# Kernel tuning notes

Measured on AMD Instinct MI355X. Metric: run time of the kernel, lower is better.

## Reference

```python
import jax, jax.numpy as jnp
import numpy as np

B, T, D = 4, 256, 1024
H, G = 512, 8
P, N, L = 384, 384, 16


def setup_inputs() -> dict:
    key = jax.random.key(0)
    ks = jax.random.split(key, 16)
    feats = jax.random.normal(ks[0], (B, T, D), jnp.float32)
    vid_idx = jnp.arange(P, dtype=jnp.int32) // (P // B)          # sorted, 96 proposals per video
    starts = jax.random.randint(ks[1], (P,), 0, T - L)
    gather_idx = jax.random.permutation(ks[2], P).astype(jnp.int32)
    block_id = jnp.repeat(jnp.arange(N // 32, dtype=jnp.int32), 32)  # 12 event sequences of 32
    s = jax.random.uniform(ks[3], (N,), minval=0.0, maxval=80.0)
    e = s + jax.random.uniform(ks[4], (N,), minval=1.0, maxval=20.0)
    timestamps = jnp.stack([s, e], axis=1)
    durations = jnp.full((N,), 120.0, jnp.float32)

    def lin(k, fi, fo):
        return jax.random.normal(k, (fi, fo), jnp.float32) / np.sqrt(fi).astype(np.float32)

    return dict(
        feats=feats, vid_idx=vid_idx, starts=starts, clip_len=L,
        gather_idx=gather_idx, block_id=block_id, timestamps=timestamps, durations=durations,
        W_pre=lin(ks[5], D, H), b_pre=jnp.zeros((H,), jnp.float32),
        W_q=lin(ks[6], H, H), b_q=jnp.zeros((H,), jnp.float32),
        W_k=lin(ks[7], H, H), b_k=jnp.zeros((H,), jnp.float32),
        W_v=lin(ks[8], H, H), b_v=jnp.zeros((H,), jnp.float32),
        W_p1=lin(ks[9], H, H), b_p1=jnp.zeros((H,), jnp.float32),
        W_p2=lin(ks[10], H, G), b_p2=jnp.zeros((G,), jnp.float32),
    )


def reference(feats, vid_idx, starts, clip_len, gather_idx, block_id, timestamps, durations,
              W_pre, b_pre, W_q, b_q, W_k, b_k, W_v, b_v, W_p1, b_p1, W_p2, b_p2):
    dt = feats.dtype
    # --- get_clip_level_feats: fixed clip_len spans -> vectorized gather ---
    t_idx = starts[:, None] + jnp.arange(clip_len)                # (P, L)
    clip_feats = feats[vid_idx[:, None], t_idx]                   # (P, L, D)
    clip_mask = jnp.ones((P, clip_len), dt)
    event_feats = clip_feats.sum(1) / (clip_mask.sum(1, keepdims=True) + 1e-5)
    # pre_map (dropout = identity in eval)
    ef = jax.nn.relu(event_feats @ W_pre + b_pre)                 # (P, H)
    # expand proposals into event rows; block-diagonal sequence mask
    X = ef[gather_idx]                                            # (N, H)
    mask = (block_id[:, None] == block_id[None, :]).astype(dt)[None]  # (1, N, N)
    # grouped scaled-dot attention
    Hg = H // G
    q = (X @ W_q + b_q).reshape(N, G, Hg).transpose(1, 0, 2)      # (G, N, Hg)
    k = (X @ W_k + b_k).reshape(N, G, Hg).transpose(1, 0, 2)
    v = (X @ W_v + b_v).reshape(N, G, Hg).transpose(1, 0, 2)
    cos_sim = jnp.einsum('gnd,gmd->gnm', q, k) / np.float32(np.sqrt(Hg))
    # --- positional relation branch ---
    st, en = timestamps[:, 0:1], timestamps[:, 1:2]               # (N, 1)
    center = 0.5 * (st + en)
    length = jnp.maximum(en - st, 0.1)
    delta_center = (center - center.T) / length                  # (N, N)
    delta_length = jnp.log(length.T / length)
    pos_mat = jnp.stack([delta_center, delta_length], axis=2)    # (N, N, 2)
    feat_range = jnp.arange(H // 4, dtype=dt)
    dim_mat = jnp.float32(10000.0) ** (4.0 / H * feat_range)      # (H/4,)
    div = (100.0 * pos_mat)[..., None] / dim_mat                  # (N, N, 2, H/4)
    pe = jnp.concatenate([jnp.sin(div), jnp.cos(div)], axis=-1).reshape(N, N, H)
    pos_sim = jnp.tanh(pe @ W_p1 + b_p1) @ W_p2 + b_p2            # (N, N, G)
    sim = cos_sim + pos_sim.transpose(2, 0, 1)                    # (G, N, N)
    sim = jax.nn.softmax(sim, axis=2)
    sim = sim * mask / (1e-5 + jnp.sum(sim * mask, axis=2, keepdims=True))
    ctx = jnp.einsum('gnm,gmd->gnd', sim, v).transpose(1, 0, 2).reshape(N, H)
    ctx = jnp.concatenate([jax.nn.relu(ctx), X], axis=1)          # (N, 2H)
    # 100-dim temporal occupancy indicator
    s_idx = jnp.minimum((timestamps[:, 0] / durations * 99).astype(jnp.int32), 99)
    e_idx = jnp.minimum((timestamps[:, 1] / durations * 99).astype(jnp.int32), 99)
    ar = jnp.arange(100)
    pos_ind = ((ar >= s_idx[:, None]) & (ar <= e_idx[:, None])).astype(dt)
    event_ctx = jnp.concatenate([ctx, pos_ind], axis=1)           # (N, 2H+100)
    return (event_ctx, clip_feats, clip_mask)
```

## Files before the change

### kernel.cpp

```cpp
#include <hip/hip_runtime.h>
#include <hip/hip_bf16.h>

#define NN 384
#define NP 147456

using short8 = __attribute__((ext_vector_type(8))) short;
using f32x4  = __attribute__((ext_vector_type(4))) float;

#define DEV static __device__ __forceinline__

DEV unsigned short f2b(float f){
  unsigned int u = __float_as_uint(f);
  u += 0x7FFFu + ((u >> 16) & 1u);
  return (unsigned short)(u >> 16);
}
DEV unsigned int pk2(float lo, float hi){
  __hip_bfloat162 h = __float22bfloat162_rn(make_float2(lo, hi));
  union { __hip_bfloat162 b; unsigned int u; } c; c.b = h; return c.u;
}
DEV float exp_e(float x){ return __builtin_amdgcn_exp2f(x * 1.4426950408889634f); }
DEV float tanh_f(float x){
  float e = exp_e(2.0f * x);
  return 1.0f - 2.0f * __builtin_amdgcn_rcpf(e + 1.0f);
}

typedef const void __attribute__((address_space(1)))* gas_ptr;
typedef void       __attribute__((address_space(3)))* las_ptr;
DEV void gload16(const void* g, void* l){
  __builtin_amdgcn_global_load_lds((gas_ptr)g, (las_ptr)l, 16, 0, 0);
}

DEV int frag_off(int r, int lane){
  return r * 64 + ((((lane >> 4) ^ ((r >> 1) & 3)) & 3) << 4);
}

__global__ __launch_bounds__(256) void setup_kernel(
    const float* __restrict__ feats, const int* __restrict__ vid_idx,
    const int* __restrict__ starts, float* __restrict__ outClip,
    float* __restrict__ outMask, unsigned short* __restrict__ evb,
    const float* __restrict__ Wpre, const float* __restrict__ Wq,
    const float* __restrict__ Wk,   const float* __restrict__ Wv,
    const float* __restrict__ W1,   const float* __restrict__ W2,
    const float* __restrict__ bq,   const float* __restrict__ bk,
    const float* __restrict__ bv,
    unsigned short* __restrict__ WTpre, unsigned short* __restrict__ WTqkv,
    unsigned short* __restrict__ W1F,   unsigned short* __restrict__ W2F,
    float* __restrict__ bqkv)
{
  __shared__ float tile[64][65];
  int bid = blockIdx.x, tid = threadIdx.x;
  if(bid < 384){
    int p = bid;
    int vid = vid_idx[p], st = starts[p];
    const float4* base = (const float4*)feats + ((long)vid * 256 + st) * 256;
    float4* oc = (float4*)outClip + (long)p * 16 * 256;
    float4 acc = make_float4(0.f, 0.f, 0.f, 0.f);
#pragma unroll
    for(int l = 0; l < 16; ++l){
      float4 v = base[l * 256 + tid];
      oc[l * 256 + tid] = v;
      acc.x += v.x; acc.y += v.y; acc.z += v.z; acc.w += v.w;
    }
    float den = 16.0f + 1e-5f;
    unsigned short* d = evb + (long)p * 1024 + tid * 4;
    d[0] = f2b(acc.x / den); d[1] = f2b(acc.y / den);
    d[2] = f2b(acc.z / den); d[3] = f2b(acc.w / den);
    if(tid < 16) outMask[p * 16 + tid] = 1.0f;
    return;
  }
  int id = bid - 384;
  if(id == 384){
    for(int i = tid; i < 8192; i += 256){
      int kk = i >> 9, l = (i >> 3) & 63, e = i & 7;
      int k = kk * 32 + ((l >> 4) << 3) + e, g = l & 15;
      W2F[i] = (g < 8) ? f2b(W2[k * 8 + g]) : (unsigned short)0;
    }
    for(int i = tid; i < 512; i += 256){
      bqkv[i] = bq[i]; bqkv[512 + i] = bk[i]; bqkv[1024 + i] = bv[i];
    }
    return;
  }
  if(id >= 320){
    int base = (id - 320) * 4096;
#pragma unroll
    for(int j = 0; j < 16; ++j){
      int i = base + j * 256 + tid;
      int e = i & 7, l = (i >> 3) & 63, cbkk = i >> 9;
      int cb = cbkk & 31, kk = cbkk >> 5;
      int k = kk * 32 + ((l >> 4) << 3) + e;
      int col = cb * 16 + (l & 15);
      W1F[i] = f2b(W1[(long)k * 512 + col]);
    }
    return;
  }
  const float* src; unsigned short* dst; int K, C, k0, c0;
  if(id < 128){ src = Wpre; dst = WTpre; K = 1024; C = 512;
                k0 = (id >> 3) * 64; c0 = (id & 7) * 64; }
  else { int l = id - 128; int which = l >> 6; int r = l & 63;
         src = which == 0 ? Wq : (which == 1 ? Wk : Wv);
         dst = WTqkv + which * 512 * 512; K = 512; C = 512;
         k0 = (r >> 3) * 64; c0 = (r & 7) * 64; }
#pragma unroll
  for(int i = 0; i < 16; ++i){
    int idx = tid + i * 256, r = idx >> 6, c = idx & 63;
    tile[r][c] = src[(long)(k0 + r) * C + c0 + c];
  }
  __syncthreads();
#pragma unroll
  for(int i = 0; i < 16; ++i){
    int idx = tid + i * 256, r = idx >> 6, c = idx & 63;
    dst[(long)(c0 + r) * K + k0 + c] = f2b(tile[c][r]);
  }
}

template<int NI>
__global__ __launch_bounds__(256, 1) void gemmN(
    const unsigned short* __restrict__ A, const int* __restrict__ gidx,
    const unsigned short* __restrict__ BT, const float* __restrict__ bias,
    float* __restrict__ Cf, unsigned short* __restrict__ Cb,
    float* __restrict__ kT, int K, int ldc, int relu)
{
  __shared__ unsigned short sA[4][64 * 32];
  __shared__ unsigned short sB[4][64 * NI * 32];
  const int tid = threadIdx.x, lane = tid & 63, w = tid >> 6;
  const int r0 = blockIdx.x * 64, c0 = blockIdx.y * (64 * NI);
  const int nk = K >> 5;

  int rA = w * 16 + (lane >> 2);
  int gsltA = (lane & 3) ^ ((rA >> 1) & 3);
  int arow = gidx ? gidx[r0 + rA] : (r0 + rA);
  const unsigned short* srcA = A + (long)arow * K + gsltA * 8;

  const unsigned short* srcB[NI];
#pragma unroll
  for(int i = 0; i < NI; ++i){
    int rB = (w * NI + i) * 16 + (lane >> 2);
    srcB[i] = BT + (long)(c0 + rB) * K + (((lane & 3) ^ ((rB >> 1) & 3)) * 8);
  }

  auto STAGE = [&](int kk){
    int buf = kk & 3, ko = kk * 32;
#pragma unroll
    for(int i = 0; i < NI; ++i)
      gload16(srcB[i] + ko, (char*)sB[buf] + (w * NI + i) * 1024);
    gload16(srcA + ko, (char*)sA[buf] + w * 1024);
  };

  f32x4 acc[4][NI];
#pragma unroll
  for(int i = 0; i < 4; ++i)
#pragma unroll
    for(int j = 0; j < NI; ++j) acc[i][j] = (f32x4){0.f, 0.f, 0.f, 0.f};

  STAGE(0); STAGE(1); STAGE(2);

  for(int kk = 0; kk < nk; ++kk){
    int cur = kk & 3;
    if constexpr(NI == 1){
      if(kk < nk - 2)       asm volatile("s_waitcnt vmcnt(4)" ::: "memory");
      else if(kk == nk - 2) asm volatile("s_waitcnt vmcnt(2)" ::: "memory");
      else                  asm volatile("s_waitcnt vmcnt(0)" ::: "memory");
    } else {
      if(kk < nk - 2)       asm volatile("s_waitcnt vmcnt(6)" ::: "memory");
      else if(kk == nk - 2) asm volatile("s_waitcnt vmcnt(3)" ::: "memory");
      else                  asm volatile("s_waitcnt vmcnt(0)" ::: "memory");
    }
    __builtin_amdgcn_s_barrier();

    short8 af[4], bfv[NI];
#pragma unroll
    for(int mi = 0; mi < 4; ++mi)
      af[mi] = *(const short8*)((const char*)sA[cur] + frag_off(mi * 16 + (lane & 15), lane));
#pragma unroll
    for(int ni = 0; ni < NI; ++ni)
      bfv[ni] = *(const short8*)((const char*)sB[cur] + frag_off(w * 16 * NI + ni * 16 + (lane & 15), lane));

    if(kk + 3 < nk) STAGE(kk + 3);

#pragma unroll
    for(int mi = 0; mi < 4; ++mi)
#pragma unroll
      for(int ni = 0; ni < NI; ++ni)
        acc[mi][ni] = __builtin_amdgcn_mfma_f32_16x16x32_bf16(af[mi], bfv[ni], acc[mi][ni], 0, 0, 0);
  }

#pragma unroll
  for(int ni = 0; ni < NI; ++ni){
    int c = c0 + w * 16 * NI + ni * 16 + (lane & 15);
    float bv = bias ? bias[c] : 0.f;
#pragma unroll
    for(int mi = 0; mi < 4; ++mi){
      int rbase = r0 + mi * 16 + ((lane >> 4) << 2);
      float4 kv4;
#pragma unroll
      for(int r = 0; r < 4; ++r){
        float v = acc[mi][ni][r] + bv;
        if(relu) v = fmaxf(v, 0.f);
        Cf[(long)(rbase + r) * ldc + c] = v;
        if(Cb) Cb[(long)(rbase + r) * ldc + c] = f2b(v);
        ((float*)&kv4)[r] = v;
      }
      if(kT && c >= 512 && c < 1024)
        *(float4*)(kT + (long)(c - 512) * 384 + rbase) = kv4;
    }
  }
}

__global__ __launch_bounds__(512, 1) void pos_sim_kernel(
    const unsigned short* __restrict__ W1F, const float* __restrict__ b1,
    const unsigned short* __restrict__ W2F, const float* __restrict__ b2,
    const float* __restrict__ ts, float* __restrict__ simc)
{
  __shared__ unsigned short peA[16][2048];
  const int tid = threadIdx.x, lane = tid & 63, w = tid >> 6;
  const int jt = tid & 7, prow = tid >> 3;
  const int swzp = (prow >> 1) & 3;

  float wj[16];
#pragma unroll
  for(int u = 0; u < 16; ++u)
    wj[u] = __builtin_amdgcn_exp2f(-0.10381025296523f * (float)(jt * 16 + u));
  float b1v[4];
#pragma unroll
  for(int ni = 0; ni < 4; ++ni) b1v[ni] = b1[w * 64 + ni * 16 + (lane & 15)];
  const float b2v = b2[lane & 7];
  const float inv2pi = 0.15915494309189535f;

  const int p0 = blockIdx.x * 64;

  {
    int q = p0 + prow;
    int n = q >> 5;
    int m = ((n >> 5) << 5) + (q & 31);
    float sn = ts[2*n], en = ts[2*n+1], sm = ts[2*m], em = ts[2*m+1];
    float cn = 0.5f*(sn+en), cm = 0.5f*(sm+em);
    float ln = fmaxf(en-sn, 0.1f), lm = fmaxf(em-sm, 0.1f);
    float a = 100.0f * (cn - cm) / ln;
    float b = 100.0f * 0.69314718055994531f * __builtin_amdgcn_logf(lm / ln);
#pragma unroll
    for(int half = 0; half < 2; ++half){
      unsigned int pa[4], pb[4], pc[4], pd[4];
#pragma unroll
      for(int up = 0; up < 4; ++up){
        int u0 = half * 8 + up * 2;
        float ra0 = __builtin_amdgcn_fractf(a * wj[u0]     * inv2pi);
        float ra1 = __builtin_amdgcn_fractf(a * wj[u0 + 1] * inv2pi);
        float rb0 = __builtin_amdgcn_fractf(b * wj[u0]     * inv2pi);
        float rb1 = __builtin_amdgcn_fractf(b * wj[u0 + 1] * inv2pi);
        pa[up] = pk2(__builtin_amdgcn_sinf(ra0), __builtin_amdgcn_sinf(ra1));
        pb[up] = pk2(__builtin_amdgcn_cosf(ra0), __builtin_amdgcn_cosf(ra1));
        pc[up] = pk2(__builtin_amdgcn_sinf(rb0), __builtin_amdgcn_sinf(rb1));
        pd[up] = pk2(__builtin_amdgcn_cosf(rb0), __builtin_amdgcn_cosf(rb1));
      }
      int s0 = (((jt & 1) * 2 + half) ^ swzp);
      char* base = (char*)&peA[0][0] + prow * 64 + (s0 << 4);
      int ch = jt >> 1;
      *(uint4*)(base + (ch     ) * 4096) = make_uint4(pa[0], pa[1], pa[2], pa[3]);
      *(uint4*)(base + (ch +  4) * 4096) = make_uint4(pb[0], pb[1], pb[2], pb[3]);
      *(uint4*)(base + (ch +  8) * 4096) = make_uint4(pc[0], pc[1], pc[2], pc[3]);
      *(uint4*)(base + (ch + 12) * 4096) = make_uint4(pd[0], pd[1], pd[2], pd[3]);
    }
  }
  asm volatile("s_waitcnt lgkmcnt(0)" ::: "memory");
  __builtin_amdgcn_s_barrier();

  f32x4 acc[4][4];
#pragma unroll
  for(int i = 0; i < 4; ++i)
#pragma unroll
    for(int j = 0; j < 4; ++j) acc[i][j] = (f32x4){0.f, 0.f, 0.f, 0.f};

  for(int kk = 0; kk < 16; ++kk){
    short8 af[4], bfv[4];
#pragma unroll
    for(int ni = 0; ni < 4; ++ni)
      bfv[ni] = *(const short8*)(W1F + (((kk * 32 + (w * 4 + ni)) * 64 + lane) << 3));
#pragma unroll
    for(int mi = 0; mi < 4; ++mi)
      af[mi] = *(const short8*)((const char*)&peA[kk][0] + frag_off(mi * 16 + (lane & 15), lane));
    __builtin_amdgcn_s_setprio(1);
#pragma unroll
    for(int mi = 0; mi < 4; ++mi)
#pragma unroll
      for(int ni = 0; ni < 4; ++ni)
        acc[mi][ni] = __builtin_amdgcn_mfma_f32_16x16x32_bf16(af[mi], bfv[ni], acc[mi][ni], 0, 0, 0);
    __builtin_amdgcn_s_setprio(0);
  }
  asm volatile("s_waitcnt lgkmcnt(0)" ::: "memory");
  __builtin_amdgcn_s_barrier();

#pragma unroll
  for(int ni = 0; ni < 4; ++ni){
    int h = w * 64 + ni * 16 + (lane & 15);
    int ch = h >> 5;
    int kb = (h & 31) * 2;
#pragma unroll
    for(int mi = 0; mi < 4; ++mi){
#pragma unroll
      for(int r = 0; r < 4; ++r){
        int row = mi * 16 + ((lane >> 4) << 2) + r;
        float tv = tanh_f(acc[mi][ni][r] + b1v[ni]);
        *(unsigned short*)((char*)&peA[ch][0] + row * 64 + (kb ^ (((row >> 1) & 3) << 4))) = f2b(tv);
      }
    }
  }
  asm volatile("s_waitcnt lgkmcnt(0)" ::: "memory");
  __builtin_amdgcn_s_barrier();

  if(w < 4){
    f32x4 acc2 = (f32x4){0.f, 0.f, 0.f, 0.f};
    for(int kk = 0; kk < 16; ++kk){
      short8 af2  = *(const short8*)((const char*)&peA[kk][0] + frag_off(w * 16 + (lane & 15), lane));
      short8 w2fk = *(const short8*)(W2F + ((kk * 64 + lane) << 3));
      acc2 = __builtin_amdgcn_mfma_f32_16x16x32_bf16(af2, w2fk, acc2, 0, 0, 0);
    }
    if((lane & 15) < 8){
      int g = lane & 15;
      int rbase = w * 16 + ((lane >> 4) << 2);
#pragma unroll
      for(int r = 0; r < 4; ++r)
        simc[(long)g * 12288 + p0 + rbase + r] = acc2[r] + b2v;
    }
  }
}

__global__ __launch_bounds__(512) void attn_tail_kernel(
    const float* __restrict__ simc, const float* __restrict__ qkv,
    const float* __restrict__ kT,
    const float* __restrict__ ef, const int* __restrict__ gidx,
    const float* __restrict__ ts, const float* __restrict__ dur,
    float* __restrict__ out)
{
  int n = blockIdx.x, tid = threadIdx.x, g = tid >> 6, lane = tid & 63;
  __shared__ float qs[8][64];
  __shared__ float w32s[8][32];
  qs[g][lane] = qkv[(long)n * 1536 + g * 64 + lane];
  __syncthreads();

  const float* srow = simc + (long)g * 12288 + (long)n * 32;
  int m0 = (n >> 5) << 5;

  float sv[6], e[6], mx = -1e30f;
#pragma unroll
  for(int i = 0; i < 6; ++i){
    int m = lane + i * 64;
    const float* kc = kT + (long)g * 24576 + m;
    float s = 0.f;
#pragma unroll 8
    for(int d = 0; d < 64; ++d)
      s = fmaf(qs[g][d], kc[(long)d * 384], s);
    float sc = (m >= m0 && m < m0 + 32) ? srow[m - m0] : 0.0f;
    sv[i] = s * 0.125f + sc;
    mx = fmaxf(mx, sv[i]);
  }
#pragma unroll
  for(int o = 32; o > 0; o >>= 1) mx = fmaxf(mx, __shfl_xor(mx, o));
  float Z = 0.f;
#pragma unroll
  for(int i = 0; i < 6; ++i){ e[i] = exp_e(sv[i] - mx); Z += e[i]; }
#pragma unroll
  for(int o = 32; o > 0; o >>= 1) Z += __shfl_xor(Z, o);
  float ms = 0.f;
#pragma unroll
  for(int i = 0; i < 6; ++i){ int m = lane + i * 64; if(m >= m0 && m < m0 + 32) ms += e[i]; }
#pragma unroll
  for(int o = 32; o > 0; o >>= 1) ms += __shfl_xor(ms, o);
  float inv = 1.0f / (1e-5f * Z + ms);
#pragma unroll
  for(int i = 0; i < 6; ++i){ int m = lane + i * 64; if(m >= m0 && m < m0 + 32) w32s[g][m - m0] = e[i] * inv; }
  __syncthreads();
  float a = 0.f;
#pragma unroll 8
  for(int j = 0; j < 32; ++j)
    a = fmaf(w32s[g][j], qkv[(long)(m0 + j) * 1536 + 1024 + g * 64 + lane], a);
  out[(long)n * 1124 + g * 64 + lane] = fmaxf(a, 0.f);

  int pidx = gidx[n];
  out[(long)n * 1124 + 512 + tid] = ef[(long)pidx * 512 + tid];
  if(tid < 100){
    float d = dur[n];
    int si = (int)(ts[2 * n]     / d * 99.0f); si = min(si, 99);
    int ei = (int)(ts[2 * n + 1] / d * 99.0f); ei = min(ei, 99);
    out[(long)n * 1124 + 1024 + tid] = (tid >= si && tid <= ei) ? 1.0f : 0.0f;
  }
}

extern "C" void kernel_launch(void* const* d_in, const int* in_sizes, int n_in,
                              void* d_out, int out_size, void* d_ws, size_t ws_size,
                              hipStream_t stream)
{
  const float* feats   = (const float*)d_in[0];
  const int*   vid_idx = (const int*)d_in[1];
  const int*   starts  = (const int*)d_in[2];
  const int*   gidx    = (const int*)d_in[4];
  const float* ts      = (const float*)d_in[6];
  const float* dur     = (const float*)d_in[7];
  const float* W_pre   = (const float*)d_in[8];
  const float* b_pre   = (const float*)d_in[9];
  const float* W_q     = (const float*)d_in[10];
  const float* b_q     = (const float*)d_in[11];
  const float* W_k     = (const float*)d_in[12];
  const float* b_k     = (const float*)d_in[13];
  const float* W_v     = (const float*)d_in[14];
  const float* b_v     = (const float*)d_in[15];
  const float* W_p1    = (const float*)d_in[16];
  const float* b_p1    = (const float*)d_in[17];
  const float* W_p2    = (const float*)d_in[18];
  const float* b_p2    = (const float*)d_in[19];

  float* out     = (float*)d_out;
  float* outClip = out + 431616;
  float* outMask = out + 6723072;

  char* ws = (char*)d_ws;
  size_t off = 0;
  auto alloc = [&](size_t bytes){ void* p = ws + off; off = (off + bytes + 255) & ~(size_t)255; return p; };
  unsigned short* evb   = (unsigned short*)alloc(384 * 1024 * 2);
  unsigned short* WTpre = (unsigned short*)alloc(512 * 1024 * 2);
  unsigned short* WTqkv = (unsigned short*)alloc((size_t)1536 * 512 * 2);
  unsigned short* W1F   = (unsigned short*)alloc(262144 * 2);
  unsigned short* W2F   = (unsigned short*)alloc(8192 * 2);
  float*  bqkv = (float*)alloc(1536 * 4);
  float*  ef   = (float*)alloc(384 * 512 * 4);
  unsigned short* efb = (unsigned short*)alloc(384 * 512 * 2);
  float*  qkv  = (float*)alloc((size_t)384 * 1536 * 4);
  float*  kT   = (float*)alloc((size_t)512 * 384 * 4);
  float*  simc = (float*)alloc((size_t)8 * 12288 * 4);

  setup_kernel<<<dim3(769), dim3(256), 0, stream>>>(
      feats, vid_idx, starts, outClip, outMask, evb,
      W_pre, W_q, W_k, W_v, W_p1, W_p2, b_q, b_k, b_v,
      WTpre, WTqkv, W1F, W2F, bqkv);
  gemmN<1><<<dim3(6, 8), dim3(256), 0, stream>>>(evb, (const int*)nullptr, WTpre, b_pre, ef, efb, (float*)nullptr, 1024, 512, 1);
  gemmN<1><<<dim3(6, 24), dim3(256), 0, stream>>>(efb, gidx, WTqkv, bqkv, qkv, (unsigned short*)nullptr, kT, 512, 1536, 0);
  pos_sim_kernel<<<dim3(192), dim3(512), 0, stream>>>(W1F, b_p1, W2F, b_p2, ts, simc);
  attn_tail_kernel<<<dim3(384), dim3(512), 0, stream>>>(simc, qkv, kT, ef, gidx, ts, dur, out);
}
```

Measured before the change: 79.58 us.

## Fuse positional-similarity MLP into attention tail kernel per query row

Merges pos_sim_kernel into attn_tail_kernel. Each of the 384 blocks now computes the sin/cos positional encodings and the two-layer tanh MLP for its own 32 block-local pairs in shared memory, then uses the scores straight from LDS. This removes one kernel launch and the global simc round trip. The cost is that each block now does 32-row MFMA tiles instead of 64-row ones, with half the waves idle in the second GEMM, and it keeps launch_bounds(512,1), which may limit occupancy of the attention part.

```diff
diff --git a/kernel.cpp b/kernel.cpp
--- a/kernel.cpp
+++ b/kernel.cpp
@@ -2,7 +2,6 @@
 #include <hip/hip_bf16.h>
 
 #define NN 384
-#define NP 147456
 
 using short8 = __attribute__((ext_vector_type(8))) short;
 using f32x4  = __attribute__((ext_vector_type(4))) float;
@@ -206,81 +205,84 @@
   }
 }
 
-__global__ __launch_bounds__(512, 1) void pos_sim_kernel(
+__global__ __launch_bounds__(512, 1) void attn_tail_kernel(
     const unsigned short* __restrict__ W1F, const float* __restrict__ b1,
     const unsigned short* __restrict__ W2F, const float* __restrict__ b2,
-    const float* __restrict__ ts, float* __restrict__ simc)
+    const float* __restrict__ qkv,  const float* __restrict__ kT,
+    const float* __restrict__ ef,   const int* __restrict__ gidx,
+    const float* __restrict__ ts,   const float* __restrict__ dur,
+    float* __restrict__ out)
 {
-  __shared__ unsigned short peA[16][2048];
-  const int tid = threadIdx.x, lane = tid & 63, w = tid >> 6;
-  const int jt = tid & 7, prow = tid >> 3;
-  const int swzp = (prow >> 1) & 3;
-
-  float wj[16];
-#pragma unroll
-  for(int u = 0; u < 16; ++u)
-    wj[u] = __builtin_amdgcn_exp2f(-0.10381025296523f * (float)(jt * 16 + u));
+  __shared__ char  peB[32768];
+  __shared__ float qs[8][64];
+  __shared__ float w32s[8][32];
+  __shared__ float scoreS[32][8];
+
+  const int n = blockIdx.x, tid = threadIdx.x;
+  const int g = tid >> 6, lane = tid & 63, w = tid >> 6, l15 = lane & 15;
+  const int m0 = (n >> 5) << 5;
+  const float kexp = -0.10381025296523f;
+  const float inv2pi = 0.15915494309189535f;
+
+  auto peAt = [&](int ch) -> char* { return peB + ch * 2048; };
+
+  qs[g][lane] = qkv[(long)n * 1536 + g * 64 + lane];
+
   float b1v[4];
 #pragma unroll
-  for(int ni = 0; ni < 4; ++ni) b1v[ni] = b1[w * 64 + ni * 16 + (lane & 15)];
-  const float b2v = b2[lane & 7];
-  const float inv2pi = 0.15915494309189535f;
-
-  const int p0 = blockIdx.x * 64;
+  for(int ni = 0; ni < 4; ++ni) b1v[ni] = b1[w * 64 + ni * 16 + l15];
 
   {
-    int q = p0 + prow;
-    int n = q >> 5;
-    int m = ((n >> 5) << 5) + (q & 31);
+    int jt = tid & 15, prow = tid >> 4;
+    int swzp = (prow >> 1) & 3;
+    int m = m0 + prow;
     float sn = ts[2*n], en = ts[2*n+1], sm = ts[2*m], em = ts[2*m+1];
     float cn = 0.5f*(sn+en), cm = 0.5f*(sm+em);
     float ln = fmaxf(en-sn, 0.1f), lm = fmaxf(em-sm, 0.1f);
     float a = 100.0f * (cn - cm) / ln;
     float b = 100.0f * 0.69314718055994531f * __builtin_amdgcn_logf(lm / ln);
-#pragma unroll
-    for(int half = 0; half < 2; ++half){
-      unsigned int pa[4], pb[4], pc[4], pd[4];
-#pragma unroll
-      for(int up = 0; up < 4; ++up){
-        int u0 = half * 8 + up * 2;
-        float ra0 = __builtin_amdgcn_fractf(a * wj[u0]     * inv2pi);
-        float ra1 = __builtin_amdgcn_fractf(a * wj[u0 + 1] * inv2pi);
-        float rb0 = __builtin_amdgcn_fractf(b * wj[u0]     * inv2pi);
-        float rb1 = __builtin_amdgcn_fractf(b * wj[u0 + 1] * inv2pi);
-        pa[up] = pk2(__builtin_amdgcn_sinf(ra0), __builtin_amdgcn_sinf(ra1));
-        pb[up] = pk2(__builtin_amdgcn_cosf(ra0), __builtin_amdgcn_cosf(ra1));
-        pc[up] = pk2(__builtin_amdgcn_sinf(rb0), __builtin_amdgcn_sinf(rb1));
-        pd[up] = pk2(__builtin_amdgcn_cosf(rb0), __builtin_amdgcn_cosf(rb1));
-      }
-      int s0 = (((jt & 1) * 2 + half) ^ swzp);
-      char* base = (char*)&peA[0][0] + prow * 64 + (s0 << 4);
-      int ch = jt >> 1;
-      *(uint4*)(base + (ch     ) * 4096) = make_uint4(pa[0], pa[1], pa[2], pa[3]);
-      *(uint4*)(base + (ch +  4) * 4096) = make_uint4(pb[0], pb[1], pb[2], pb[3]);
-      *(uint4*)(base + (ch +  8) * 4096) = make_uint4(pc[0], pc[1], pc[2], pc[3]);
-      *(uint4*)(base + (ch + 12) * 4096) = make_uint4(pd[0], pd[1], pd[2], pd[3]);
-    }
+    unsigned int pa[4], pb[4], pc[4], pd[4];
+#pragma unroll
+    for(int e2 = 0; e2 < 4; ++e2){
+      int j0 = jt * 8 + e2 * 2;
+      float w0 = __builtin_amdgcn_exp2f(kexp * (float)j0);
+      float w1 = __builtin_amdgcn_exp2f(kexp * (float)(j0 + 1));
+      float ra0 = __builtin_amdgcn_fractf(a * w0 * inv2pi);
+      float ra1 = __builtin_amdgcn_fractf(a * w1 * inv2pi);
+      float rb0 = __builtin_amdgcn_fractf(b * w0 * inv2pi);
+      float rb1 = __builtin_amdgcn_fractf(b * w1 * inv2pi);
+      pa[e2] = pk2(__builtin_amdgcn_sinf(ra0), __builtin_amdgcn_sinf(ra1));
+      pb[e2] = pk2(__builtin_amdgcn_cosf(ra0), __builtin_amdgcn_cosf(ra1));
+      pc[e2] = pk2(__builtin_amdgcn_sinf(rb0), __builtin_amdgcn_sinf(rb1));
+      pd[e2] = pk2(__builtin_amdgcn_cosf(rb0), __builtin_amdgcn_cosf(rb1));
+    }
+    int lowoff = prow * 64 + ((((jt & 3) ^ swzp)) << 4);
+    int ch = jt >> 2;
+    *(uint4*)(peAt(ch     ) + lowoff) = make_uint4(pa[0], pa[1], pa[2], pa[3]);
+    *(uint4*)(peAt(ch +  4) + lowoff) = make_uint4(pb[0], pb[1], pb[2], pb[3]);
+    *(uint4*)(peAt(ch +  8) + lowoff) = make_uint4(pc[0], pc[1], pc[2], pc[3]);
+    *(uint4*)(peAt(ch + 12) + lowoff) = make_uint4(pd[0], pd[1], pd[2], pd[3]);
   }
   asm volatile("s_waitcnt lgkmcnt(0)" ::: "memory");
   __builtin_amdgcn_s_barrier();
 
-  f32x4 acc[4][4];
-#pragma unroll
-  for(int i = 0; i < 4; ++i)
+  f32x4 acc[2][4];
+#pragma unroll
+  for(int i = 0; i < 2; ++i)
 #pragma unroll
     for(int j = 0; j < 4; ++j) acc[i][j] = (f32x4){0.f, 0.f, 0.f, 0.f};
 
   for(int kk = 0; kk < 16; ++kk){
-    short8 af[4], bfv[4];
+    short8 af[2], bfv[4];
 #pragma unroll
     for(int ni = 0; ni < 4; ++ni)
       bfv[ni] = *(const short8*)(W1F + (((kk * 32 + (w * 4 + ni)) * 64 + lane) << 3));
 #pragma unroll
-    for(int mi = 0; mi < 4; ++mi)
-      af[mi] = *(const short8*)((const char*)&peA[kk][0] + frag_off(mi * 16 + (lane & 15), lane));
+    for(int mi = 0; mi < 2; ++mi)
+      af[mi] = *(const short8*)(peAt(kk) + frag_off(mi * 16 + l15, lane));
     __builtin_amdgcn_s_setprio(1);
 #pragma unroll
-    for(int mi = 0; mi < 4; ++mi)
+    for(int mi = 0; mi < 2; ++mi)
 #pragma unroll
       for(int ni = 0; ni < 4; ++ni)
         acc[mi][ni] = __builtin_amdgcn_mfma_f32_16x16x32_bf16(af[mi], bfv[ni], acc[mi][ni], 0, 0, 0);
@@ -291,54 +293,40 @@
 
 #pragma unroll
   for(int ni = 0; ni < 4; ++ni){
-    int h = w * 64 + ni * 16 + (lane & 15);
+    int h = w * 64 + ni * 16 + l15;
     int ch = h >> 5;
     int kb = (h & 31) * 2;
 #pragma unroll
-    for(int mi = 0; mi < 4; ++mi){
+    for(int mi = 0; mi < 2; ++mi){
 #pragma unroll
       for(int r = 0; r < 4; ++r){
         int row = mi * 16 + ((lane >> 4) << 2) + r;
         float tv = tanh_f(acc[mi][ni][r] + b1v[ni]);
-        *(unsigned short*)((char*)&peA[ch][0] + row * 64 + (kb ^ (((row >> 1) & 3) << 4))) = f2b(tv);
+        *(unsigned short*)(peAt(ch) + row * 64 + (kb ^ (((row >> 1) & 3) << 4))) = f2b(tv);
       }
     }
   }
   asm volatile("s_waitcnt lgkmcnt(0)" ::: "memory");
   __builtin_amdgcn_s_barrier();
 
-  if(w < 4){
+  if(w < 2){
     f32x4 acc2 = (f32x4){0.f, 0.f, 0.f, 0.f};
     for(int kk = 0; kk < 16; ++kk){
-      short8 af2  = *(const short8*)((const char*)&peA[kk][0] + frag_off(w * 16 + (lane & 15), lane));
+      short8 af2  = *(const short8*)(peAt(kk) + frag_off(w * 16 + l15, lane));
       short8 w2fk = *(const short8*)(W2F + ((kk * 64 + lane) << 3));
       acc2 = __builtin_amdgcn_mfma_f32_16x16x32_bf16(af2, w2fk, acc2, 0, 0, 0);
     }
-    if((lane & 15) < 8){
-      int g = lane & 15;
+    if(l15 < 8){
+      int g2 = l15;
+      float b2v = b2[g2];
       int rbase = w * 16 + ((lane >> 4) << 2);
 #pragma unroll
       for(int r = 0; r < 4; ++r)
-        simc[(long)g * 12288 + p0 + rbase + r] = acc2[r] + b2v;
-    }
-  }
-}
-
-__global__ __launch_bounds__(512) void attn_tail_kernel(
-    const float* __restrict__ simc, const float* __restrict__ qkv,
-    const float* __restrict__ kT,
-    const float* __restrict__ ef, const int* __restrict__ gidx,
-    const float* __restrict__ ts, const float* __restrict__ dur,
-    float* __restrict__ out)
-{
-  int n = blockIdx.x, tid = threadIdx.x, g = tid >> 6, lane = tid & 63;
-  __shared__ float qs[8][64];
-  __shared__ float w32s[8][32];
-  qs[g][lane] = qkv[(long)n * 1536 + g * 64 + lane];
-  __syncthreads();
-
-  const float* srow = simc + (long)g * 12288 + (long)n * 32;
-  int m0 = (n >> 5) << 5;
+        scoreS[rbase + r][g2] = acc2[r] + b2v;
+    }
+  }
+  asm volatile("s_waitcnt lgkmcnt(0)" ::: "memory");
+  __builtin_amdgcn_s_barrier();
 
   float sv[6], e[6], mx = -1e30f;
 #pragma unroll
@@ -349,7 +337,7 @@
 #pragma unroll 8
     for(int d = 0; d < 64; ++d)
       s = fmaf(qs[g][d], kc[(long)d * 384], s);
-    float sc = (m >= m0 && m < m0 + 32) ? srow[m - m0] : 0.0f;
+    float sc = (m >= m0 && m < m0 + 32) ? scoreS[m - m0][g] : 0.0f;
     sv[i] = s * 0.125f + sc;
     mx = fmaxf(mx, sv[i]);
   }
@@ -425,7 +413,6 @@
   unsigned short* efb = (unsigned short*)alloc(384 * 512 * 2);
   float*  qkv  = (float*)alloc((size_t)384 * 1536 * 4);
   float*  kT   = (float*)alloc((size_t)512 * 384 * 4);
-  float*  simc = (float*)alloc((size_t)8 * 12288 * 4);
 
   setup_kernel<<<dim3(769), dim3(256), 0, stream>>>(
       feats, vid_idx, starts, outClip, outMask, evb,
@@ -433,6 +420,6 @@
       WTpre, WTqkv, W1F, W2F, bqkv);
   gemmN<1><<<dim3(6, 8), dim3(256), 0, stream>>>(evb, (const int*)nullptr, WTpre, b_pre, ef, efb, (float*)nullptr, 1024, 512, 1);
   gemmN<1><<<dim3(6, 24), dim3(256), 0, stream>>>(efb, gidx, WTqkv, bqkv, qkv, (unsigned short*)nullptr, kT, 512, 1536, 0);
-  pos_sim_kernel<<<dim3(192), dim3(512), 0, stream>>>(W1F, b_p1, W2F, b_p2, ts, simc);
-  attn_tail_kernel<<<dim3(384), dim3(512), 0, stream>>>(simc, qkv, kT, ef, gidx, ts, dur, out);
-}
+  attn_tail_kernel<<<dim3(384), dim3(512), 0, stream>>>(
+      W1F, b_p1, W2F, b_p2, qkv, kT, ef, gidx, ts, dur, out);
+}
```

Measured after the change: 76.40 us. 1.04x faster.
